# Kernel tuning notes

Hardware: AMD Instinct MI355X
Metric: run time of the kernel (lower is better)

Reference implementation:

```python
import jax, jax.numpy as jnp
import numpy as np

B, T, D = 8, 2048, 1024
E, S = 8, 1            # num_experts, num_slots
FF = 4 * (S * D)       # ffn_mult * (num_slots * hiddens)

def setup_inputs() -> dict:
    key = jax.random.key(0)
    ks = jax.random.split(key, 7)
    sd = S * D
    inp = {
        "X":  jax.random.normal(ks[0], (B, T, D), dtype=jnp.float32),
        # slots gating MLP (single linear D -> E*S)
        "Wg": jax.random.normal(ks[1], (D, E * S), dtype=jnp.float32) / np.sqrt(D),
        "bg": jnp.zeros((E * S,), dtype=jnp.float32),
        # expert FFN (weights SHARED across experts, as in source [FFN(...)]*E)
        "W1": jax.random.normal(ks[2], (sd, FF), dtype=jnp.float32) / np.sqrt(sd),
        "b1": jnp.zeros((FF,), dtype=jnp.float32),
        "W2": jax.random.normal(ks[3], (FF, sd), dtype=jnp.float32) / np.sqrt(FF),
        "b2": jnp.zeros((sd,), dtype=jnp.float32),
    }
    return inp

def reference(X, Wg, bg, W1, b1, W2, b2):
    # logits: (B, T, E*S)
    logits = jnp.einsum('btd,de->bte', X, Wg) + bg
    dispatch_w = jax.nn.softmax(logits, axis=1)   # over tokens T
    combine_w = jax.nn.softmax(logits, axis=2)    # over slots E*S
    # slots = dispatch_w^T @ X : (B, E*S, D) -> (B, E, S*D)
    slots = jnp.einsum('bte,btd->bed', dispatch_w, X).reshape(B, E, S * D)
    # shared-weight FFN applied per expert slot (dropout=0 at eval)
    h = jax.nn.silu(jnp.einsum('bef,fh->beh', slots, W1) + b1)
    y = jnp.einsum('beh,hf->bef', h, W2) + b2     # (B, E, S*D)
    y = y.reshape(B, E * S, D)
    # combine: (B, T, E*S) @ (B, E*S, D)
    return jnp.einsum('bte,bed->btd', combine_w, y)
```

## Files before the change

kernel.cpp:

```cpp
#include <hip/hip_runtime.h>
#include <math.h>

#define B_  8
#define T_  2048
#define D_  1024
#define E_  8
#define FF_ 4096
#define N_  64
#define BT_ (B_*T_)
#define WGS 1028

__global__ __launch_bounds__(256) void k_logits(
    const float* __restrict__ X, const float* __restrict__ Wg,
    const float* __restrict__ bg, float* __restrict__ logits,
    float* __restrict__ sumexp)
{
    __shared__ float wgT[E_ * WGS];
    __shared__ float xt[32 * 132];
    __shared__ float red[256];

    const int tid = threadIdx.x;

    #pragma unroll
    for (int r = 0; r < 32; ++r) {
        int idx = r * 256 + tid;
        wgT[(idx & 7) * WGS + (idx >> 3)] = Wg[idx];
    }

    const int bt0 = blockIdx.x * 32;
    const int tok = tid >> 3;
    const int e   = tid & 7;
    float acc = 0.f;

    for (int dt = 0; dt < 8; ++dt) {
        __syncthreads();
        #pragma unroll
        for (int r = 0; r < 4; ++r) {
            int idx4 = r * 256 + tid;
            int row = idx4 >> 5, c4 = idx4 & 31;
            const float4 v = *(const float4*)&X[(size_t)(bt0 + row) * D_ + dt * 128 + c4 * 4];
            *(float4*)&xt[row * 132 + c4 * 4] = v;
        }
        __syncthreads();
        const float4* xp = (const float4*)&xt[tok * 132];
        const float4* wp = (const float4*)&wgT[e * WGS + dt * 128];
        #pragma unroll
        for (int j = 0; j < 32; ++j) {
            const float4 xv = xp[j];
            const float4 wv = wp[j];
            acc += xv.x * wv.x + xv.y * wv.y + xv.z * wv.z + xv.w * wv.w;
        }
    }

    const float lg = acc + bg[e];
    logits[(size_t)(bt0 + tok) * E_ + e] = lg;

    red[tid] = expf(lg);
    __syncthreads();
    for (int s = 128; s >= 8; s >>= 1) {
        if (tid < s) red[tid] += red[tid + s];
        __syncthreads();
    }
    if (tid < 8) {
        atomicAdd(&sumexp[(bt0 >> 11) * E_ + tid], red[tid]);
    }
}

__global__ __launch_bounds__(256) void k_slots_part(
    const float* __restrict__ X, const float* __restrict__ logits,
    const float* __restrict__ sumexp, float* __restrict__ part)
{
    __shared__ float wlds[64 * 8];
    __shared__ float inv[8];

    const int tid = threadIdx.x;
    const int ts = blockIdx.x, b = blockIdx.y;
    const int t0 = ts * 64;

    if (tid < 8) inv[tid] = 1.f / sumexp[b * E_ + tid];
    __syncthreads();
    #pragma unroll
    for (int r = 0; r < 2; ++r) {
        int idx = r * 256 + tid;
        wlds[idx] = expf(logits[(size_t)b * T_ * E_ + (size_t)t0 * E_ + idx]) * inv[idx & 7];
    }
    __syncthreads();

    float4 acc[8];
    #pragma unroll
    for (int e = 0; e < 8; ++e) { acc[e].x = acc[e].y = acc[e].z = acc[e].w = 0.f; }

    const float* xb = &X[((size_t)b * T_ + t0) * D_ + tid * 4];
    #pragma unroll 4
    for (int t = 0; t < 64; ++t) {
        const float4 x4 = *(const float4*)&xb[(size_t)t * D_];
        const float4 wA = *(const float4*)&wlds[t * 8];
        const float4 wB = *(const float4*)&wlds[t * 8 + 4];
        const float w[8] = {wA.x, wA.y, wA.z, wA.w, wB.x, wB.y, wB.z, wB.w};
        #pragma unroll
        for (int e = 0; e < 8; ++e) {
            acc[e].x += x4.x * w[e];
            acc[e].y += x4.y * w[e];
            acc[e].z += x4.z * w[e];
            acc[e].w += x4.w * w[e];
        }
    }
    #pragma unroll
    for (int e = 0; e < 8; ++e) {
        *(float4*)&part[(size_t)ts * (N_ * D_) + (size_t)(b * E_ + e) * D_ + tid * 4] = acc[e];
    }
}

__global__ __launch_bounds__(256) void k_reduce_slots(
    const float* __restrict__ part, float* __restrict__ slots)
{
    const int i = blockIdx.x * 256 + threadIdx.x;
    float s = 0.f;
    #pragma unroll
    for (int p = 0; p < 32; ++p) s += part[(size_t)p * (N_ * D_) + i];
    slots[i] = s;
}

__global__ __launch_bounds__(256) void k_gemm_part(
    const float* __restrict__ A, const float* __restrict__ W,
    float* __restrict__ part, int K, int F)
{
    __shared__ float sT[32 * 68];

    const int tid = threadIdx.x;
    const int f0 = blockIdx.x * 512 + tid;
    const int k0 = blockIdx.y * 32;

    #pragma unroll
    for (int r = 0; r < 8; ++r) {
        int idx = r * 256 + tid;
        int n = idx >> 5, kk = idx & 31;
        sT[kk * 68 + n] = A[(size_t)n * K + k0 + kk];
    }
    __syncthreads();

    float acc0[64], acc1[64];
    #pragma unroll
    for (int n = 0; n < 64; ++n) { acc0[n] = 0.f; acc1[n] = 0.f; }

    #pragma unroll 4
    for (int kk = 0; kk < 32; ++kk) {
        const float w0 = W[(size_t)(k0 + kk) * F + f0];
        const float w1 = W[(size_t)(k0 + kk) * F + f0 + 256];
        const float4* sp = (const float4*)&sT[kk * 68];
        #pragma unroll
        for (int j = 0; j < 16; ++j) {
            const float4 s = sp[j];
            acc0[4*j+0] += s.x * w0; acc0[4*j+1] += s.y * w0;
            acc0[4*j+2] += s.z * w0; acc0[4*j+3] += s.w * w0;
            acc1[4*j+0] += s.x * w1; acc1[4*j+1] += s.y * w1;
            acc1[4*j+2] += s.z * w1; acc1[4*j+3] += s.w * w1;
        }
    }

    const size_t base = (size_t)blockIdx.y * N_ * F;
    #pragma unroll
    for (int n = 0; n < 64; ++n) {
        part[base + (size_t)n * F + f0]       = acc0[n];
        part[base + (size_t)n * F + f0 + 256] = acc1[n];
    }
}

__global__ __launch_bounds__(256) void k_reduce_silu(
    const float* __restrict__ part, const float* __restrict__ b1,
    float* __restrict__ h)
{
    const int i = blockIdx.x * 256 + threadIdx.x;
    float s = 0.f;
    #pragma unroll
    for (int p = 0; p < 32; ++p) s += part[(size_t)p * (N_ * FF_) + i];
    s += b1[i & (FF_ - 1)];
    h[i] = s / (1.f + expf(-s));
}

__global__ __launch_bounds__(256) void k_reduce_bias(
    const float* __restrict__ part, const float* __restrict__ b2,
    float* __restrict__ y)
{
    const int i = blockIdx.x * 256 + threadIdx.x;
    float s = 0.f;
    #pragma unroll
    for (int p = 0; p < 128; ++p) s += part[(size_t)p * (N_ * D_) + i];
    y[i] = s + b2[i & (D_ - 1)];
}

__global__ __launch_bounds__(256) void k_combine(
    const float* __restrict__ logits, const float* __restrict__ y,
    float* __restrict__ out)
{
    __shared__ float wlds[64 * 8];
    const int tid = threadIdx.x;
    const int dc = blockIdx.x, tc = blockIdx.y, b = blockIdx.z;
    const int t0 = tc * 64;

    if (tid < 64) {
        const float* lp = &logits[((size_t)b * T_ + t0 + tid) * E_];
        float ex[8]; float s = 0.f;
        #pragma unroll
        for (int i = 0; i < 8; ++i) { ex[i] = expf(lp[i]); s += ex[i]; }
        const float invs = 1.f / s;
        #pragma unroll
        for (int i = 0; i < 8; ++i) wlds[tid * 8 + i] = ex[i] * invs;
    }
    __syncthreads();

    const int d = dc * 256 + tid;
    float yv[8];
    #pragma unroll
    for (int e = 0; e < 8; ++e) yv[e] = y[(size_t)(b * E_ + e) * D_ + d];

    for (int t = 0; t < 64; ++t) {
        const float4 wA = *(const float4*)&wlds[t * 8];
        const float4 wB = *(const float4*)&wlds[t * 8 + 4];
        const float acc = wA.x * yv[0] + wA.y * yv[1] + wA.z * yv[2] + wA.w * yv[3]
                        + wB.x * yv[4] + wB.y * yv[5] + wB.z * yv[6] + wB.w * yv[7];
        out[((size_t)b * T_ + t0 + t) * D_ + d] = acc;
    }
}

extern "C" void kernel_launch(void* const* d_in, const int* in_sizes, int n_in,
                              void* d_out, int out_size, void* d_ws, size_t ws_size,
                              hipStream_t stream)
{
    const float* X  = (const float*)d_in[0];
    const float* Wg = (const float*)d_in[1];
    const float* bg = (const float*)d_in[2];
    const float* W1 = (const float*)d_in[3];
    const float* b1 = (const float*)d_in[4];
    const float* W2 = (const float*)d_in[5];
    const float* b2 = (const float*)d_in[6];
    float* out = (float*)d_out;

    float* wsf    = (float*)d_ws;
    float* logits = wsf;
    float* sumexp = logits + BT_ * E_;
    float* slots  = sumexp + 64;
    float* h      = slots + N_ * D_;
    float* y      = h + N_ * FF_;

    float* part = out;

    hipMemsetAsync(sumexp, 0, 64 * sizeof(float), stream);

    hipLaunchKernelGGL(k_logits,       dim3(BT_ / 32), dim3(256), 0, stream,
                       X, Wg, bg, logits, sumexp);
    hipLaunchKernelGGL(k_slots_part,   dim3(32, 8),    dim3(256), 0, stream,
                       X, logits, sumexp, part);
    hipLaunchKernelGGL(k_reduce_slots, dim3(256),      dim3(256), 0, stream,
                       part, slots);
    hipLaunchKernelGGL(k_gemm_part,    dim3(FF_ / 512, 1024 / 32), dim3(256), 0, stream,
                       slots, W1, part, 1024, FF_);
    hipLaunchKernelGGL(k_reduce_silu,  dim3(N_ * FF_ / 256), dim3(256), 0, stream,
                       part, b1, h);
    hipLaunchKernelGGL(k_gemm_part,    dim3(D_ / 512, FF_ / 32), dim3(256), 0, stream,
                       h, W2, part, FF_, D_);
    hipLaunchKernelGGL(k_reduce_bias,  dim3(N_ * D_ / 256), dim3(256), 0, stream,
                       part, b2, y);
    hipLaunchKernelGGL(k_combine,      dim3(4, 32, 8), dim3(256), 0, stream,
                       logits, y, out);
}
```

Measured before the change: 271.8 us.

## Restructure logits kernel with register-held weights and tune slots/combine kernels

The logits kernel now keeps the gating weights in registers per wave, streams X rows with prefetch, and reduces via wave shuffles instead of an LDS tile and tree reduction. The slots partial kernel is split finer (32 tokens per block, 64 partials), and the combine kernel is vectorised to float4 per thread, with one block covering all of D. Fast __expf replaces expf in several places and the GEMM unroll is raised. The aim is less LDS traffic and fewer syncs in logits and more parallelism elsewhere. In exchange the logits kernel uses many more registers, and the finer split doubles the partial-reduction reads.

```diff
diff --git a/kernel.cpp b/kernel.cpp
--- a/kernel.cpp
+++ b/kernel.cpp
@@ -16,74 +16,95 @@
     float* __restrict__ sumexp)
 {
     __shared__ float wgT[E_ * WGS];
-    __shared__ float xt[32 * 132];
-    __shared__ float red[256];
-
-    const int tid = threadIdx.x;
+
+    const int tid  = threadIdx.x;
+    const int lane = tid & 63;
+    const int wv   = tid >> 6;
 
     #pragma unroll
     for (int r = 0; r < 32; ++r) {
         int idx = r * 256 + tid;
         wgT[(idx & 7) * WGS + (idx >> 3)] = Wg[idx];
     }
-
-    const int bt0 = blockIdx.x * 32;
-    const int tok = tid >> 3;
-    const int e   = tid & 7;
-    float acc = 0.f;
-
-    for (int dt = 0; dt < 8; ++dt) {
-        __syncthreads();
-        #pragma unroll
-        for (int r = 0; r < 4; ++r) {
-            int idx4 = r * 256 + tid;
-            int row = idx4 >> 5, c4 = idx4 & 31;
-            const float4 v = *(const float4*)&X[(size_t)(bt0 + row) * D_ + dt * 128 + c4 * 4];
-            *(float4*)&xt[row * 132 + c4 * 4] = v;
-        }
-        __syncthreads();
-        const float4* xp = (const float4*)&xt[tok * 132];
-        const float4* wp = (const float4*)&wgT[e * WGS + dt * 128];
-        #pragma unroll
-        for (int j = 0; j < 32; ++j) {
-            const float4 xv = xp[j];
-            const float4 wv = wp[j];
-            acc += xv.x * wv.x + xv.y * wv.y + xv.z * wv.z + xv.w * wv.w;
-        }
-    }
-
-    const float lg = acc + bg[e];
-    logits[(size_t)(bt0 + tok) * E_ + e] = lg;
-
-    red[tid] = expf(lg);
-    __syncthreads();
-    for (int s = 128; s >= 8; s >>= 1) {
-        if (tid < s) red[tid] += red[tid + s];
-        __syncthreads();
-    }
-    if (tid < 8) {
-        atomicAdd(&sumexp[(bt0 >> 11) * E_ + tid], red[tid]);
-    }
+    __syncthreads();
+
+    float4 w4[4][8];
+    #pragma unroll
+    for (int j = 0; j < 4; ++j)
+        #pragma unroll
+        for (int e = 0; e < 8; ++e)
+            w4[j][e] = *(const float4*)&wgT[e * WGS + j * 256 + lane * 4];
+
+    const int t0 = blockIdx.x * 64 + wv * 16;
+    const int b  = t0 >> 11;
+    const float bgv = bg[lane & 7];
+
+    float se = 0.f;
+    const float* xrow = &X[(size_t)t0 * D_ + lane * 4];
+
+    float4 xc[4];
+    #pragma unroll
+    for (int j = 0; j < 4; ++j) xc[j] = *(const float4*)&xrow[j * 256];
+
+    for (int t = 0; t < 16; ++t) {
+        float4 xn[4];
+        if (t < 15) {
+            #pragma unroll
+            for (int j = 0; j < 4; ++j)
+                xn[j] = *(const float4*)&xrow[(size_t)(t + 1) * D_ + j * 256];
+        }
+        float acc[8];
+        #pragma unroll
+        for (int e = 0; e < 8; ++e) acc[e] = 0.f;
+        #pragma unroll
+        for (int j = 0; j < 4; ++j) {
+            const float4 x = xc[j];
+            #pragma unroll
+            for (int e = 0; e < 8; ++e) {
+                const float4 w = w4[j][e];
+                acc[e] += x.x * w.x + x.y * w.y + x.z * w.z + x.w * w.w;
+            }
+        }
+        #pragma unroll
+        for (int j = 0; j < 4; ++j) xc[j] = xn[j];
+
+        #pragma unroll
+        for (int e = 0; e < 8; ++e) {
+            acc[e] += __shfl_xor(acc[e], 1);
+            acc[e] += __shfl_xor(acc[e], 2);
+            acc[e] += __shfl_xor(acc[e], 4);
+        }
+        const float a01 = (lane & 1) ? acc[1] : acc[0];
+        const float a23 = (lane & 1) ? acc[3] : acc[2];
+        const float a45 = (lane & 1) ? acc[5] : acc[4];
+        const float a67 = (lane & 1) ? acc[7] : acc[6];
+        const float a03 = (lane & 2) ? a23 : a01;
+        const float a47 = (lane & 2) ? a67 : a45;
+        float v = (lane & 4) ? a47 : a03;
+        v += __shfl_xor(v, 8);
+        v += __shfl_xor(v, 16);
+        v += __shfl_xor(v, 32);
+        v += bgv;
+        if (lane < 8) logits[(size_t)(t0 + t) * E_ + lane] = v;
+        se += __expf(v);
+    }
+    if (lane < 8) atomicAdd(&sumexp[b * E_ + lane], se);
 }
 
 __global__ __launch_bounds__(256) void k_slots_part(
     const float* __restrict__ X, const float* __restrict__ logits,
     const float* __restrict__ sumexp, float* __restrict__ part)
 {
-    __shared__ float wlds[64 * 8];
+    __shared__ float wlds[32 * 8];
     __shared__ float inv[8];
 
     const int tid = threadIdx.x;
     const int ts = blockIdx.x, b = blockIdx.y;
-    const int t0 = ts * 64;
+    const int t0 = ts * 32;
 
     if (tid < 8) inv[tid] = 1.f / sumexp[b * E_ + tid];
     __syncthreads();
-    #pragma unroll
-    for (int r = 0; r < 2; ++r) {
-        int idx = r * 256 + tid;
-        wlds[idx] = expf(logits[(size_t)b * T_ * E_ + (size_t)t0 * E_ + idx]) * inv[idx & 7];
-    }
+    wlds[tid] = __expf(logits[(size_t)b * T_ * E_ + (size_t)t0 * E_ + tid]) * inv[tid & 7];
     __syncthreads();
 
     float4 acc[8];
@@ -91,8 +112,8 @@
     for (int e = 0; e < 8; ++e) { acc[e].x = acc[e].y = acc[e].z = acc[e].w = 0.f; }
 
     const float* xb = &X[((size_t)b * T_ + t0) * D_ + tid * 4];
-    #pragma unroll 4
-    for (int t = 0; t < 64; ++t) {
+    #pragma unroll 8
+    for (int t = 0; t < 32; ++t) {
         const float4 x4 = *(const float4*)&xb[(size_t)t * D_];
         const float4 wA = *(const float4*)&wlds[t * 8];
         const float4 wB = *(const float4*)&wlds[t * 8 + 4];
@@ -117,7 +138,7 @@
     const int i = blockIdx.x * 256 + threadIdx.x;
     float s = 0.f;
     #pragma unroll
-    for (int p = 0; p < 32; ++p) s += part[(size_t)p * (N_ * D_) + i];
+    for (int p = 0; p < 64; ++p) s += part[(size_t)p * (N_ * D_) + i];
     slots[i] = s;
 }
 
@@ -143,7 +164,7 @@
     #pragma unroll
     for (int n = 0; n < 64; ++n) { acc0[n] = 0.f; acc1[n] = 0.f; }
 
-    #pragma unroll 4
+    #pragma unroll 8
     for (int kk = 0; kk < 32; ++kk) {
         const float w0 = W[(size_t)(k0 + kk) * F + f0];
         const float w1 = W[(size_t)(k0 + kk) * F + f0 + 256];
@@ -175,7 +196,7 @@
     #pragma unroll
     for (int p = 0; p < 32; ++p) s += part[(size_t)p * (N_ * FF_) + i];
     s += b1[i & (FF_ - 1)];
-    h[i] = s / (1.f + expf(-s));
+    h[i] = s / (1.f + __expf(-s));
 }
 
 __global__ __launch_bounds__(256) void k_reduce_bias(
@@ -195,31 +216,39 @@
 {
     __shared__ float wlds[64 * 8];
     const int tid = threadIdx.x;
-    const int dc = blockIdx.x, tc = blockIdx.y, b = blockIdx.z;
+    const int tc = blockIdx.x, b = blockIdx.y;
     const int t0 = tc * 64;
 
     if (tid < 64) {
         const float* lp = &logits[((size_t)b * T_ + t0 + tid) * E_];
         float ex[8]; float s = 0.f;
         #pragma unroll
-        for (int i = 0; i < 8; ++i) { ex[i] = expf(lp[i]); s += ex[i]; }
+        for (int i = 0; i < 8; ++i) { ex[i] = __expf(lp[i]); s += ex[i]; }
         const float invs = 1.f / s;
         #pragma unroll
         for (int i = 0; i < 8; ++i) wlds[tid * 8 + i] = ex[i] * invs;
     }
     __syncthreads();
 
-    const int d = dc * 256 + tid;
-    float yv[8];
-    #pragma unroll
-    for (int e = 0; e < 8; ++e) yv[e] = y[(size_t)(b * E_ + e) * D_ + d];
-
+    float4 yv[8];
+    #pragma unroll
+    for (int e = 0; e < 8; ++e)
+        yv[e] = *(const float4*)&y[(size_t)(b * E_ + e) * D_ + tid * 4];
+
+    #pragma unroll 4
     for (int t = 0; t < 64; ++t) {
         const float4 wA = *(const float4*)&wlds[t * 8];
         const float4 wB = *(const float4*)&wlds[t * 8 + 4];
-        const float acc = wA.x * yv[0] + wA.y * yv[1] + wA.z * yv[2] + wA.w * yv[3]
-                        + wB.x * yv[4] + wB.y * yv[5] + wB.z * yv[6] + wB.w * yv[7];
-        out[((size_t)b * T_ + t0 + t) * D_ + d] = acc;
+        float4 a;
+        a.x = wA.x*yv[0].x + wA.y*yv[1].x + wA.z*yv[2].x + wA.w*yv[3].x
+            + wB.x*yv[4].x + wB.y*yv[5].x + wB.z*yv[6].x + wB.w*yv[7].x;
+        a.y = wA.x*yv[0].y + wA.y*yv[1].y + wA.z*yv[2].y + wA.w*yv[3].y
+            + wB.x*yv[4].y + wB.y*yv[5].y + wB.z*yv[6].y + wB.w*yv[7].y;
+        a.z = wA.x*yv[0].z + wA.y*yv[1].z + wA.z*yv[2].z + wA.w*yv[3].z
+            + wB.x*yv[4].z + wB.y*yv[5].z + wB.z*yv[6].z + wB.w*yv[7].z;
+        a.w = wA.x*yv[0].w + wA.y*yv[1].w + wA.z*yv[2].w + wA.w*yv[3].w
+            + wB.x*yv[4].w + wB.y*yv[5].w + wB.z*yv[6].w + wB.w*yv[7].w;
+        *(float4*)&out[((size_t)b * T_ + t0 + t) * D_ + tid * 4] = a;
     }
 }
 
@@ -247,9 +276,9 @@
 
     hipMemsetAsync(sumexp, 0, 64 * sizeof(float), stream);
 
-    hipLaunchKernelGGL(k_logits,       dim3(BT_ / 32), dim3(256), 0, stream,
+    hipLaunchKernelGGL(k_logits,       dim3(BT_ / 64), dim3(256), 0, stream,
                        X, Wg, bg, logits, sumexp);
-    hipLaunchKernelGGL(k_slots_part,   dim3(32, 8),    dim3(256), 0, stream,
+    hipLaunchKernelGGL(k_slots_part,   dim3(64, 8),    dim3(256), 0, stream,
                        X, logits, sumexp, part);
     hipLaunchKernelGGL(k_reduce_slots, dim3(256),      dim3(256), 0, stream,
                        part, slots);
@@ -261,6 +290,6 @@
                        h, W2, part, FF_, D_);
     hipLaunchKernelGGL(k_reduce_bias,  dim3(N_ * D_ / 256), dim3(256), 0, stream,
                        part, b2, y);
-    hipLaunchKernelGGL(k_combine,      dim3(4, 32, 8), dim3(256), 0, stream,
+    hipLaunchKernelGGL(k_combine,      dim3(32, 8), dim3(256), 0, stream,
                        logits, y, out);
 }
```

Result: slower. 285.9 us (+5.2%).
